# Kernel tuning notes

Measured on AMD Instinct MI355X. Metric: run time of the kernel, lower is better.

The kernel has to match this reference:

```python
import jax, jax.numpy as jnp
import numpy as np

DN = ('NHWC', 'HWIO', 'NHWC')

def conv(x, w, stride=1):
    return jax.lax.conv_general_dilated(x, w, (stride, stride), 'SAME', dimension_numbers=DN)

def up2(x):
    return jnp.repeat(jnp.repeat(x, 2, axis=1), 2, axis=2)

def nms(boxes, scores, max_output=100, iou_thresh=0.5):
    # greedy sequential NMS, fixed trip count, padded outputs
    NEG = jnp.float32(-1e30)
    area = (boxes[:, 2] - boxes[:, 0]) * (boxes[:, 3] - boxes[:, 1])  # [N]
    def step(sw, _):
        idx = jnp.argmax(sw)
        s = sw[idx]
        b = boxes[idx]
        valid = s > NEG * 0.5
        y1 = jnp.maximum(b[0], boxes[:, 0]); x1 = jnp.maximum(b[1], boxes[:, 1])
        y2 = jnp.minimum(b[2], boxes[:, 2]); x2 = jnp.minimum(b[3], boxes[:, 3])
        inter = jnp.maximum(y2 - y1, 0.0) * jnp.maximum(x2 - x1, 0.0)
        barea = (b[2] - b[0]) * (b[3] - b[1])
        iou = inter / (barea + area - inter + 1e-9)
        sw = jnp.where(iou > iou_thresh, NEG, sw)  # suppress (includes self)
        out_b = jnp.where(valid, b, jnp.zeros(4, boxes.dtype))
        out_s = jnp.where(valid, s, jnp.float32(0.0))
        return sw, (out_b, out_s)
    _, (sel_boxes, sel_scores) = jax.lax.scan(step, scores, None, length=max_output)
    return sel_boxes, sel_scores

def setup_inputs() -> dict:
    key = jax.random.key(0)
    ks = jax.random.split(key, 16)
    def w(k, shape):
        fan_in = shape[0] * shape[1] * shape[2]
        return jax.random.normal(k, shape, jnp.float32) * jnp.sqrt(2.0 / fan_in)
    return {
        'inputs': jax.random.normal(ks[0], (1, 512, 512, 3), jnp.float32),
        # backbone (resnet50-style channel widths, strides 2/4/8/16/32)
        'w_stem': w(ks[1], (7, 7, 3, 64)),
        'w_c2': w(ks[2], (3, 3, 64, 256)),
        'w_c3': w(ks[3], (3, 3, 256, 512)),
        'w_c4': w(ks[4], (3, 3, 512, 1024)),
        'w_c5': w(ks[5], (3, 3, 1024, 2048)),
        # FPN laterals + output convs (channels=256)
        'l3': w(ks[6], (1, 1, 512, 256)),
        'l4': w(ks[7], (1, 1, 1024, 256)),
        'l5': w(ks[8], (1, 1, 2048, 256)),
        'o3': w(ks[9], (3, 3, 256, 256)),
        'o4': w(ks[10], (3, 3, 256, 256)),
        'o5': w(ks[11], (3, 3, 256, 256)),
        # RPN: shared 3x3 + obj head (num_anchors=1) + bbox head (4*num_anchors)
        'w_rpn': w(ks[12], (3, 3, 256, 256)),
        'w_obj': w(ks[13], (1, 1, 256, 1)),
        'w_box': w(ks[14], (1, 1, 256, 4)),
    }

def reference(inputs, w_stem, w_c2, w_c3, w_c4, w_c5, l3, l4, l5, o3, o4, o5, w_rpn, w_obj, w_box):
    relu = jax.nn.relu
    # backbone
    s = relu(conv(inputs, w_stem, 2))   # 256x256x64
    c2 = relu(conv(s, w_c2, 2))         # 128x128x256
    c3 = relu(conv(c2, w_c3, 2))        # 64x64x512
    c4 = relu(conv(c3, w_c4, 2))        # 32x32x1024
    c5 = relu(conv(c4, w_c5, 2))        # 16x16x2048
    # FPN
    p5 = conv(c5, l5)
    p4 = conv(c4, l4) + up2(p5)
    p3 = conv(c3, l3) + up2(p4)
    p3, p4, p5 = conv(p3, o3), conv(p4, o4), conv(p5, o5)
    # RPN over all levels (bbox deltas computed per original but unused downstream)
    obj_logits = []
    for p in (p3, p4, p5):
        t = relu(conv(p, w_rpn))
        obj_logits.append(conv(t, w_obj))
        _ = conv(t, w_box)
    obj = obj_logits[0]  # [B, h, w, A]
    B, h, w_, A = obj.shape
    scores = jax.nn.sigmoid(obj).reshape(B, -1)  # [B, h*w*A]
    # anchor grid (fixed 0.1-sized boxes), faithful to TF meshgrid default 'xy' indexing
    yy = jnp.linspace(0.0, 1.0, h)
    xx = jnp.linspace(0.0, 1.0, w_)
    Y, X = jnp.meshgrid(yy, xx)  # shape [w, h]
    boxes = jnp.stack([Y - 0.05, X - 0.05, Y + 0.05, X + 0.05], axis=-1)
    boxes = jnp.clip(boxes, 0.0, 1.0).reshape(-1, 4)  # [w*h, 4]
    sel_boxes, sel_scores = nms(boxes, scores[0], max_output=100, iou_thresh=0.5)
    return sel_boxes, sel_scores
```

## Files before the change

kernel.cpp:

```cpp
#include <hip/hip_runtime.h>
#include <hip/hip_bf16.h>

typedef float f4 __attribute__((ext_vector_type(4)));
typedef short s8v __attribute__((ext_vector_type(8)));
typedef unsigned short us4 __attribute__((ext_vector_type(4)));
typedef unsigned short us8 __attribute__((ext_vector_type(8)));

#define AP 40

__global__ __launch_bounds__(256) void stem_kernel(
    const float* __restrict__ in, const float* __restrict__ w,
    float* __restrict__ out)
{
  __shared__ float in_lds[37 * 37 * 3];
  __shared__ float w_lds[7 * 7 * 3 * 64];
  const int tid = threadIdx.x;
  const int ty0 = (blockIdx.x >> 4) * 16;
  const int tx0 = (blockIdx.x & 15) * 16;

  for (int idx = tid; idx < 9408; idx += 256) w_lds[idx] = w[idx];
  for (int idx = tid; idx < 4107; idx += 256) {
    int ci = idx % 3;
    int rem = idx / 3;
    int ix = rem % 37, iy = rem / 37;
    int gy = ty0 * 2 - 2 + iy, gx = tx0 * 2 - 2 + ix;
    float v = 0.f;
    if ((unsigned)gy < 512u && (unsigned)gx < 512u)
      v = in[(gy * 512 + gx) * 3 + ci];
    in_lds[idx] = v;
  }
  __syncthreads();

  const int co = (tid & 15) * 4;
  const int py = tid >> 4;
  f4 acc[16];
#pragma unroll
  for (int px = 0; px < 16; ++px) acc[px] = (f4)0.f;

  for (int ky = 0; ky < 7; ++ky)
    for (int kx = 0; kx < 7; ++kx)
#pragma unroll
      for (int ci = 0; ci < 3; ++ci) {
        f4 wv = *(const f4*)&w_lds[(((ky * 7 + kx) * 3) + ci) * 64 + co];
        const float* ip = &in_lds[((2 * py + ky) * 37 + kx) * 3 + ci];
#pragma unroll
        for (int px = 0; px < 16; ++px) {
          float iv = ip[px * 6];
          acc[px] += iv * wv;
        }
      }

#pragma unroll
  for (int px = 0; px < 16; ++px) {
    int oy = ty0 + py, ox = tx0 + px;
    f4 o = acc[px];
#pragma unroll
    for (int c = 0; c < 4; ++c) o[c] = fmaxf(o[c], 0.f);
    *(f4*)&out[(oy * 256 + ox) * 64 + co] = o;
  }
}

__global__ __launch_bounds__(256) void wsplit_kernel(
    const float* __restrict__ w, unsigned short* __restrict__ wt,
    int C_in, int C_out, int taps)
{
  __shared__ float t[64][68];
  const int tid = threadIdx.x;
  const int tap = blockIdx.z;
  const int ci0 = blockIdx.x * 64;
  const int co0 = blockIdx.y * 64;
  const size_t lstride = (size_t)taps * C_in * C_out;

#pragma unroll
  for (int q = 0; q < 4; ++q) {
    int f = q * 256 + tid;
    int r = f >> 4, c = f & 15;
    f4 v = *(const f4*)&w[((size_t)(tap * C_in + ci0 + r)) * C_out + co0 + c * 4];
    *(f4*)&t[r][c * 4] = v;
  }
  __syncthreads();

#pragma unroll
  for (int q = 0; q < 4; ++q) {
    int f = q * 256 + tid;
    int r = f >> 4, c = f & 15;
    us4 h, m, l;
#pragma unroll
    for (int u = 0; u < 4; ++u) {
      float s = t[c * 4 + u][r];
      unsigned int ub = __float_as_uint(s);
      unsigned short hh = (unsigned short)(ub >> 16);
      float r1 = s - __uint_as_float((unsigned int)hh << 16);
      unsigned short mm = (unsigned short)(__float_as_uint(r1) >> 16);
      float r2 = r1 - __uint_as_float((unsigned int)mm << 16);
      unsigned short ll = (unsigned short)(__float_as_uint(r2) >> 16);
      h[u] = hh; m[u] = mm; l[u] = ll;
    }
    size_t base = ((size_t)tap * C_out + co0 + r) * C_in + ci0 + c * 4;
    *(us4*)&wt[base] = h;
    *(us4*)&wt[lstride + base] = m;
    *(us4*)&wt[2 * lstride + base] = l;
  }
}

__global__ __launch_bounds__(256, 2) void conv_mfma(
    const float* __restrict__ in, const unsigned short* __restrict__ wt,
    float* __restrict__ pout,
    int H_in, int W_in, int C_in, int wshift, int C_out,
    int stride, int pad, int ci_per_z, int npix, int relu)
{
  __shared__ __align__(16) unsigned short At[3][128][AP];
  __shared__ __align__(16) unsigned short Bt[3][128][AP];
  const int tid = threadIdx.x;

  const int nwg = gridDim.x * gridDim.y * gridDim.z;
  const int hwid = blockIdx.x + gridDim.x * (blockIdx.y + gridDim.y * blockIdx.z);
  const int wid = ((nwg & 7) == 0) ? (hwid & 7) * (nwg >> 3) + (hwid >> 3) : hwid;
  const int bx = wid % gridDim.x;
  const int brem = wid / gridDim.x;
  const int by = brem % gridDim.y;
  const int bz = brem / gridDim.y;

  const int pix_base = bx * 128;
  const int co_base = by * 128;
  const int ci_z0 = bz * ci_per_z;
  const int wmask = (1 << wshift) - 1;
  const size_t lstride = (size_t)9 * C_in * C_out;

  const int lane = tid & 63, wv = tid >> 6;
  const int pixhalf = (wv >> 1) * 64, cohalf = (wv & 1) * 64;
  const int fm = lane & 15, fq = lane >> 4;

  int a_pix[4], a_c4[4], a_ys[4], a_xs[4];
#pragma unroll
  for (int q = 0; q < 4; ++q) {
    int f = q * 256 + tid;
    a_pix[q] = f >> 3; a_c4[q] = f & 7;
    int p = pix_base + a_pix[q];
    a_ys[q] = (p >> wshift) * stride - pad;
    a_xs[q] = (p & wmask) * stride - pad;
  }
  int b_col[2], b_seg[2];
#pragma unroll
  for (int q = 0; q < 2; ++q) {
    int f = q * 256 + tid;
    b_col[q] = f >> 2; b_seg[q] = (f & 3) * 8;
  }

  const int nc = ci_per_z >> 5;
  const int ncsh = nc >> 1;
  const int nchunks = 9 * nc;

  f4 areg[4];
  us8 breg[6];
  auto issue_loads = [&](int c) {
    int tap = c >> ncsh;
    int ci = ci_z0 + (c & (nc - 1)) * 32;
    int ky = tap / 3, kx = tap - ky * 3;
#pragma unroll
    for (int q = 0; q < 4; ++q) {
      int iy = a_ys[q] + ky, ix = a_xs[q] + kx;
      bool v = ((unsigned)iy < (unsigned)H_in) & ((unsigned)ix < (unsigned)W_in);
      const float* p = in + (size_t)(iy * W_in + ix) * C_in + ci + a_c4[q] * 4;
      areg[q] = v ? *(const f4*)p : (f4)0.f;
    }
    const unsigned short* bb =
        wt + (size_t)tap * C_out * C_in + (size_t)co_base * C_in + ci;
#pragma unroll
    for (int L = 0; L < 3; ++L)
#pragma unroll
      for (int q = 0; q < 2; ++q)
        breg[L * 2 + q] = *(const us8*)(bb + (size_t)L * lstride +
                                        (size_t)b_col[q] * C_in + b_seg[q]);
  };

  us4 ah[4], am[4], al[4];
  auto convert = [&]() {
#pragma unroll
    for (int q = 0; q < 4; ++q) {
      f4 s4 = areg[q];
      us4 h, m, l;
#pragma unroll
      for (int u = 0; u < 4; ++u) {
        float s = s4[u];
        unsigned int ub = __float_as_uint(s);
        unsigned short hh = (unsigned short)(ub >> 16);
        float r1 = s - __uint_as_float((unsigned int)hh << 16);
        unsigned short mm = (unsigned short)(__float_as_uint(r1) >> 16);
        float r2 = r1 - __uint_as_float((unsigned int)mm << 16);
        unsigned short ll = (unsigned short)(__float_as_uint(r2) >> 16);
        h[u] = hh; m[u] = mm; l[u] = ll;
      }
      ah[q] = h; am[q] = m; al[q] = l;
    }
  };

  f4 acc[4][4];
#pragma unroll
  for (int i = 0; i < 4; ++i)
#pragma unroll
    for (int j = 0; j < 4; ++j) acc[i][j] = (f4)0.f;

  issue_loads(0);
  convert();

  for (int c = 0; c < nchunks; ++c) {
    __syncthreads();
#pragma unroll
    for (int q = 0; q < 4; ++q) {
      *(us4*)&At[0][a_pix[q]][a_c4[q] * 4] = ah[q];
      *(us4*)&At[1][a_pix[q]][a_c4[q] * 4] = am[q];
      *(us4*)&At[2][a_pix[q]][a_c4[q] * 4] = al[q];
    }
#pragma unroll
    for (int L = 0; L < 3; ++L)
#pragma unroll
      for (int q = 0; q < 2; ++q)
        *(us8*)&Bt[L][b_col[q]][b_seg[q]] = breg[L * 2 + q];
    __syncthreads();

    const bool more = (c + 1 < nchunks);
    if (more) issue_loads(c + 1);

    s8v Bh[4], Bm[4], Bl[4];
#pragma unroll
    for (int j = 0; j < 4; ++j) {
      Bh[j] = *(const s8v*)&Bt[0][cohalf + j * 16 + fm][fq * 8];
      Bm[j] = *(const s8v*)&Bt[1][cohalf + j * 16 + fm][fq * 8];
      Bl[j] = *(const s8v*)&Bt[2][cohalf + j * 16 + fm][fq * 8];
    }
    {
      s8v Ah[4];
#pragma unroll
      for (int i = 0; i < 4; ++i)
        Ah[i] = *(const s8v*)&At[0][pixhalf + i * 16 + fm][fq * 8];
#pragma unroll
      for (int i = 0; i < 4; ++i)
#pragma unroll
        for (int j = 0; j < 4; ++j) {
          acc[i][j] = __builtin_amdgcn_mfma_f32_16x16x32_bf16(Ah[i], Bh[j], acc[i][j], 0, 0, 0);
          acc[i][j] = __builtin_amdgcn_mfma_f32_16x16x32_bf16(Ah[i], Bm[j], acc[i][j], 0, 0, 0);
          acc[i][j] = __builtin_amdgcn_mfma_f32_16x16x32_bf16(Ah[i], Bl[j], acc[i][j], 0, 0, 0);
        }
    }
    {
      s8v Am[4];
#pragma unroll
      for (int i = 0; i < 4; ++i)
        Am[i] = *(const s8v*)&At[1][pixhalf + i * 16 + fm][fq * 8];
#pragma unroll
      for (int i = 0; i < 4; ++i)
#pragma unroll
        for (int j = 0; j < 4; ++j) {
          acc[i][j] = __builtin_amdgcn_mfma_f32_16x16x32_bf16(Am[i], Bh[j], acc[i][j], 0, 0, 0);
          acc[i][j] = __builtin_amdgcn_mfma_f32_16x16x32_bf16(Am[i], Bm[j], acc[i][j], 0, 0, 0);
        }
    }
    {
      s8v Al[4];
#pragma unroll
      for (int i = 0; i < 4; ++i)
        Al[i] = *(const s8v*)&At[2][pixhalf + i * 16 + fm][fq * 8];
#pragma unroll
      for (int i = 0; i < 4; ++i)
#pragma unroll
        for (int j = 0; j < 4; ++j)
          acc[i][j] = __builtin_amdgcn_mfma_f32_16x16x32_bf16(Al[i], Bh[j], acc[i][j], 0, 0, 0);
    }

    if (more) convert();
  }

  float* dst = pout + (size_t)bz * npix * C_out;
#pragma unroll
  for (int i = 0; i < 4; ++i) {
#pragma unroll
    for (int j = 0; j < 4; ++j) {
#pragma unroll
      for (int r = 0; r < 4; ++r) {
        int p = pix_base + pixhalf + i * 16 + fq * 4 + r;
        int co = co_base + cohalf + j * 16 + fm;
        float v = acc[i][j][r];
        if (relu) v = fmaxf(v, 0.f);
        dst[(size_t)p * C_out + co] = v;
      }
    }
  }
}

__global__ __launch_bounds__(256) void reduce_relu_kernel(
    const float* __restrict__ p, float* __restrict__ out, int n4, int Z, int relu)
{
  int idx = blockIdx.x * 256 + threadIdx.x;
  if (idx >= n4) return;
  const f4* pv = (const f4*)p;
  f4 s = pv[idx];
  for (int z = 1; z < Z; ++z) s += pv[(size_t)z * n4 + idx];
  if (relu) {
#pragma unroll
    for (int c = 0; c < 4; ++c) s[c] = fmaxf(s[c], 0.f);
  }
  ((f4*)out)[idx] = s;
}

__global__ __launch_bounds__(256) void gemm64(
    const float* __restrict__ in, const float* __restrict__ w,
    float* __restrict__ pout, int C_in, int C_out, int ci_per_z, int npix)
{
  __shared__ __align__(16) float As2[32][68];
  __shared__ __align__(16) float Bs[32][64];
  const int tid = threadIdx.x;
  const int pix_base = blockIdx.x * 64;
  const int co_base = blockIdx.y * 64;
  const int ci_z0 = blockIdx.z * ci_per_z;
  const int tx = tid & 15, ty = tid >> 4;

  int ga_pix[2], ga_c4[2];
#pragma unroll
  for (int q = 0; q < 2; ++q) {
    int f = q * 256 + tid;
    ga_pix[q] = f >> 3; ga_c4[q] = f & 7;
  }
  int gb_row[2], gb_c4[2];
#pragma unroll
  for (int q = 0; q < 2; ++q) {
    int f = q * 256 + tid;
    gb_row[q] = f >> 4; gb_c4[q] = f & 15;
  }

  f4 acc[4];
#pragma unroll
  for (int i = 0; i < 4; ++i) acc[i] = (f4)0.f;

  for (int ci = ci_z0; ci < ci_z0 + ci_per_z; ci += 32) {
    __syncthreads();
#pragma unroll
    for (int q = 0; q < 2; ++q) {
      f4 av = *(const f4*)&in[(size_t)(pix_base + ga_pix[q]) * C_in + ci + ga_c4[q] * 4];
#pragma unroll
      for (int u = 0; u < 4; ++u) As2[ga_c4[q] * 4 + u][ga_pix[q]] = av[u];
    }
#pragma unroll
    for (int q = 0; q < 2; ++q) {
      *(f4*)&Bs[gb_row[q]][gb_c4[q] * 4] =
          *(const f4*)&w[(size_t)(ci + gb_row[q]) * C_out + co_base + gb_c4[q] * 4];
    }
    __syncthreads();
#pragma unroll
    for (int kk = 0; kk < 32; ++kk) {
      f4 a = *(const f4*)&As2[kk][ty * 4];
      f4 b = *(const f4*)&Bs[kk][tx * 4];
#pragma unroll
      for (int i = 0; i < 4; ++i) acc[i] += a[i] * b;
    }
  }

  float* dst = pout + (size_t)blockIdx.z * npix * C_out;
#pragma unroll
  for (int i = 0; i < 4; ++i)
    *(f4*)&dst[(size_t)(pix_base + ty * 4 + i) * C_out + co_base + tx * 4] = acc[i];
}

__global__ __launch_bounds__(256) void reduce_up2_kernel(
    const float* __restrict__ p, const float* __restrict__ res,
    float* __restrict__ out, int n4, int Z, int wshift)
{
  int idx = blockIdx.x * 256 + threadIdx.x;
  if (idx >= n4) return;
  const f4* pv = (const f4*)p;
  f4 s = pv[idx];
  for (int z = 1; z < Z; ++z) s += pv[(size_t)z * n4 + idx];
  if (res) {
    int pix = idx >> 6, c4 = idx & 63;
    int oy = pix >> wshift, ox = pix & ((1 << wshift) - 1);
    int rp = ((oy >> 1) << (wshift - 1)) + (ox >> 1);
    s += ((const f4*)res)[rp * 64 + c4];
  }
  ((f4*)out)[idx] = s;
}

__global__ __launch_bounds__(256) void obj_sigmoid_kernel(
    const float* __restrict__ t, const float* __restrict__ wobj,
    float* __restrict__ scores)
{
  __shared__ float wl[256];
  const int tid = threadIdx.x;
  wl[tid] = wobj[tid];
  __syncthreads();
  const int pix = blockIdx.x * 64 + (tid >> 2);
  const int c0 = (tid & 3) * 64;
  float acc = 0.f;
#pragma unroll
  for (int k = 0; k < 16; ++k) {
    f4 tv = *(const f4*)&t[(size_t)pix * 256 + c0 + k * 4];
    const float* wp = &wl[c0 + k * 4];
    acc += tv[0] * wp[0] + tv[1] * wp[1] + tv[2] * wp[2] + tv[3] * wp[3];
  }
  acc += __shfl_xor(acc, 1);
  acc += __shfl_xor(acc, 2);
  if ((tid & 3) == 0) scores[pix] = 1.f / (1.f + expf(-acc));
}

__global__ __launch_bounds__(1024) void nms_kernel(
    const float* __restrict__ scores, float* __restrict__ out)
{
  __shared__ unsigned long long keys[4096];
  __shared__ float acc_lds[100 * 8];
  const int tid = threadIdx.x;
  const float inv63 = 1.0f / 63.0f;

  if (tid < 125) ((f4*)out)[tid] = (f4)0.f;

#pragma unroll
  for (int r = 0; r < 4; ++r) {
    int idx = r * 1024 + tid;
    unsigned int bits = __float_as_uint(scores[idx]);
    keys[idx] = ((unsigned long long)(0x40000000u - bits) << 16) |
                (unsigned long long)idx;
  }

  int prev_cross = 1;
  for (int k = 2; k <= 4096; k <<= 1) {
    for (int j = k >> 1; j > 0; j >>= 1) {
      const int cross = (j > 32);
      if (cross | prev_cross) {
        __syncthreads();
      } else {
        asm volatile("s_waitcnt lgkmcnt(0)" ::: "memory");
      }
#pragma unroll
      for (int q = 0; q < 2; ++q) {
        int p = q * 1024 + tid;
        int i = ((p & ~(j - 1)) << 1) | (p & (j - 1));
        int partner = i | j;
        bool up = ((i & k) == 0);
        unsigned long long a = keys[i], b = keys[partner];
        if ((a > b) == up) { keys[i] = b; keys[partner] = a; }
      }
      prev_cross = cross;
    }
  }
  __syncthreads();

  if (tid >= 64) return;
  const int lane = tid;

  int n = 0;
  for (int b = 0; b < 64 && n < 100; ++b) {
    unsigned long long kk = keys[b * 64 + lane];
    int idx = (int)(kk & 0xFFFF);
    float sc = __uint_as_float(0x40000000u - (unsigned int)(kk >> 16));
    int si = idx >> 6, sj = idx & 63;
    float y = sj * inv63, x = si * inv63;
    float c0 = fmaxf(y - 0.05f, 0.f), c1 = fmaxf(x - 0.05f, 0.f);
    float c2 = fminf(y + 0.05f, 1.f), c3 = fminf(x + 0.05f, 1.f);
    float carea = (c2 - c0) * (c3 - c1);

    bool sup = false;
    for (int a = 0; a < n; ++a) {
      f4 ab = *(const f4*)&acc_lds[a * 8];
      float aarea = acc_lds[a * 8 + 4];
      float yy1 = fmaxf(ab[0], c0), xx1 = fmaxf(ab[1], c1);
      float yy2 = fminf(ab[2], c2), xx2 = fminf(ab[3], c3);
      float inter = fmaxf(yy2 - yy1, 0.f) * fmaxf(xx2 - xx1, 0.f);
      float iou = inter / (aarea + carea - inter + 1e-9f);
      sup = sup || (iou > 0.5f);
    }

    unsigned long long m = __ballot(!sup);
    while (m != 0 && n < 100) {
      int u = __builtin_ctzll(m);
      float b0 = __shfl(c0, u), b1 = __shfl(c1, u);
      float b2 = __shfl(c2, u), b3 = __shfl(c3, u);
      float ba = __shfl(carea, u);
      if (lane == u) {
        acc_lds[n * 8 + 0] = c0; acc_lds[n * 8 + 1] = c1;
        acc_lds[n * 8 + 2] = c2; acc_lds[n * 8 + 3] = c3;
        acc_lds[n * 8 + 4] = carea;
        out[n * 4 + 0] = c0; out[n * 4 + 1] = c1;
        out[n * 4 + 2] = c2; out[n * 4 + 3] = c3;
        out[400 + n] = sc;
        sup = true;
      }
      n++;
      if (lane > u && !sup) {
        float yy1 = fmaxf(b0, c0), xx1 = fmaxf(b1, c1);
        float yy2 = fminf(b2, c2), xx2 = fminf(b3, c3);
        float inter = fmaxf(yy2 - yy1, 0.f) * fmaxf(xx2 - xx1, 0.f);
        float iou = inter / (ba + carea - inter + 1e-9f);
        if (iou > 0.5f) sup = true;
      }
      m = __ballot(!sup);
    }
    __threadfence_block();
  }
}

extern "C" void kernel_launch(void* const* d_in, const int* in_sizes, int n_in,
                              void* d_out, int out_size, void* d_ws, size_t ws_size,
                              hipStream_t stream) {
  const float* x      = (const float*)d_in[0];
  const float* w_stem = (const float*)d_in[1];
  const float* w_c2   = (const float*)d_in[2];
  const float* w_c3   = (const float*)d_in[3];
  const float* w_c4   = (const float*)d_in[4];
  const float* w_c5   = (const float*)d_in[5];
  const float* l3     = (const float*)d_in[6];
  const float* l4     = (const float*)d_in[7];
  const float* l5     = (const float*)d_in[8];
  const float* o3w    = (const float*)d_in[9];
  const float* w_rpn  = (const float*)d_in[12];
  const float* w_obj  = (const float*)d_in[13];
  float* out = (float*)d_out;
  float* ws = (float*)d_ws;

  float* S   = ws;
  float* C2  = S   + 4194304;
  float* C3  = C2  + 4194304;
  float* C4  = C3  + 2097152;
  float* C5  = C4  + 1048576;
  float* P5  = C5  + 524288;
  float* P4  = P5  + 65536;
  float* P3P = P4  + 262144;
  float* P3  = P3P + 1048576;
  float* T   = P3  + 1048576;
  float* SC  = T   + 1048576;
  unsigned short* WT = (unsigned short*)(SC + 4096);
  float* PZ = (float*)(WT + 31457280);

  stem_kernel<<<256, 256, 0, stream>>>(x, w_stem, S);

  wsplit_kernel<<<dim3(1, 4, 9), 256, 0, stream>>>(w_c2, WT, 64, 256, 9);
  conv_mfma<<<dim3(128, 2, 2), 256, 0, stream>>>(
      S, WT, PZ, 256, 256, 64, 7, 256, 2, 0, 32, 16384, 0);
  reduce_relu_kernel<<<4096, 256, 0, stream>>>(PZ, C2, 1048576, 2, 1);

  wsplit_kernel<<<dim3(4, 8, 9), 256, 0, stream>>>(w_c3, WT, 256, 512, 9);
  conv_mfma<<<dim3(32, 4, 4), 256, 0, stream>>>(
      C2, WT, PZ, 128, 128, 256, 6, 512, 2, 0, 64, 4096, 0);
  reduce_relu_kernel<<<2048, 256, 0, stream>>>(PZ, C3, 524288, 4, 1);

  wsplit_kernel<<<dim3(8, 16, 9), 256, 0, stream>>>(w_c4, WT, 512, 1024, 9);
  conv_mfma<<<dim3(8, 8, 8), 256, 0, stream>>>(
      C3, WT, S, 64, 64, 512, 5, 1024, 2, 0, 64, 1024, 0);
  reduce_relu_kernel<<<1024, 256, 0, stream>>>(S, C4, 262144, 8, 1);

  wsplit_kernel<<<dim3(16, 32, 9), 256, 0, stream>>>(w_c5, WT, 1024, 2048, 9);
  conv_mfma<<<dim3(2, 16, 16), 256, 0, stream>>>(
      C4, WT, S, 32, 32, 1024, 4, 2048, 2, 0, 64, 256, 0);
  reduce_relu_kernel<<<512, 256, 0, stream>>>(S, C5, 131072, 16, 1);

  gemm64<<<dim3(4, 4, 8), 256, 0, stream>>>(C5, l5, S, 2048, 256, 256, 256);
  reduce_up2_kernel<<<64, 256, 0, stream>>>(S, nullptr, P5, 16384, 8, 4);
  gemm64<<<dim3(16, 4, 4), 256, 0, stream>>>(C4, l4, S, 1024, 256, 256, 1024);
  reduce_up2_kernel<<<256, 256, 0, stream>>>(S, P5, P4, 65536, 4, 5);
  gemm64<<<dim3(64, 4, 2), 256, 0, stream>>>(C3, l3, S, 512, 256, 256, 4096);
  reduce_up2_kernel<<<1024, 256, 0, stream>>>(S, P4, P3P, 262144, 2, 6);

  wsplit_kernel<<<dim3(4, 4, 9), 256, 0, stream>>>(o3w, WT, 256, 256, 9);
  conv_mfma<<<dim3(32, 2, 8), 256, 0, stream>>>(
      P3P, WT, S, 64, 64, 256, 6, 256, 1, 1, 32, 4096, 0);
  reduce_relu_kernel<<<1024, 256, 0, stream>>>(S, P3, 262144, 8, 0);

  wsplit_kernel<<<dim3(4, 4, 9), 256, 0, stream>>>(w_rpn, WT, 256, 256, 9);
  conv_mfma<<<dim3(32, 2, 8), 256, 0, stream>>>(
      P3, WT, S, 64, 64, 256, 6, 256, 1, 1, 32, 4096, 0);
  reduce_relu_kernel<<<1024, 256, 0, stream>>>(S, T, 262144, 8, 1);

  obj_sigmoid_kernel<<<64, 256, 0, stream>>>(T, w_obj, SC);
  nms_kernel<<<1, 1024, 0, stream>>>(SC, out);
}
```

Before: 640.6 us.

## Register-resident bitonic sort in NMS using shuffles for small strides

Rewrites the bitonic sort in the NMS kernel so each thread holds four keys in registers. Stages with stride 4 to 128 use cross-lane shuffles, strides 1 and 2 are compared inside the thread, and only strides of 256 or more go through LDS with barriers. This is meant to cut the many LDS round-trips and block-wide syncs of the old shared-memory sort. The tradeoff is that 64-bit shuffles take two instructions each and register use goes up.

```diff
diff --git a/kernel.cpp b/kernel.cpp
--- a/kernel.cpp
+++ b/kernel.cpp
@@ -411,35 +411,75 @@
 
   if (tid < 125) ((f4*)out)[tid] = (f4)0.f;
 
-#pragma unroll
-  for (int r = 0; r < 4; ++r) {
-    int idx = r * 1024 + tid;
-    unsigned int bits = __float_as_uint(scores[idx]);
-    keys[idx] = ((unsigned long long)(0x40000000u - bits) << 16) |
-                (unsigned long long)idx;
-  }
-
-  int prev_cross = 1;
+  unsigned long long kr[4];
+  {
+    f4 sv = ((const f4*)scores)[tid];
+#pragma unroll
+    for (int v = 0; v < 4; ++v) {
+      unsigned int bits = __float_as_uint(sv[v]);
+      kr[v] = ((unsigned long long)(0x40000000u - bits) << 16) |
+              (unsigned long long)(tid * 4 + v);
+    }
+  }
+
   for (int k = 2; k <= 4096; k <<= 1) {
-    for (int j = k >> 1; j > 0; j >>= 1) {
-      const int cross = (j > 32);
-      if (cross | prev_cross) {
-        __syncthreads();
-      } else {
-        asm volatile("s_waitcnt lgkmcnt(0)" ::: "memory");
-      }
-#pragma unroll
-      for (int q = 0; q < 2; ++q) {
-        int p = q * 1024 + tid;
-        int i = ((p & ~(j - 1)) << 1) | (p & (j - 1));
-        int partner = i | j;
-        bool up = ((i & k) == 0);
-        unsigned long long a = keys[i], b = keys[partner];
-        if ((a > b) == up) { keys[i] = b; keys[partner] = a; }
-      }
-      prev_cross = cross;
-    }
-  }
+    for (int j = k >> 1; j >= 256; j >>= 1) {
+      *(ulonglong2*)&keys[tid * 4] = ulonglong2{kr[0], kr[1]};
+      *(ulonglong2*)&keys[tid * 4 + 2] = ulonglong2{kr[2], kr[3]};
+      __syncthreads();
+      ulonglong2 p0 = *(const ulonglong2*)&keys[(tid * 4) ^ j];
+      ulonglong2 p1 = *(const ulonglong2*)&keys[((tid * 4) ^ j) + 2];
+      unsigned long long pb[4] = {p0.x, p0.y, p1.x, p1.y};
+#pragma unroll
+      for (int v = 0; v < 4; ++v) {
+        int e = tid * 4 + v;
+        bool up = ((e & k) == 0);
+        bool lower = ((e & j) == 0);
+        bool keep_min = (lower == up);
+        unsigned long long a = kr[v], b = pb[v];
+        unsigned long long mn = a < b ? a : b;
+        unsigned long long mx = a < b ? b : a;
+        kr[v] = keep_min ? mn : mx;
+      }
+      __syncthreads();
+    }
+    {
+      int js = (k >> 1) < 128 ? (k >> 1) : 128;
+      for (int j = js; j >= 4; j >>= 1) {
+        int lm = j >> 2;
+        bool lower = ((tid & lm) == 0);
+        bool up = ((tid & (k >> 2)) == 0);
+        bool keep_min = (lower == up);
+#pragma unroll
+        for (int v = 0; v < 4; ++v) {
+          unsigned long long b = __shfl_xor(kr[v], lm);
+          unsigned long long a = kr[v];
+          unsigned long long mn = a < b ? a : b;
+          unsigned long long mx = a < b ? b : a;
+          kr[v] = keep_min ? mn : mx;
+        }
+      }
+    }
+    if (k >= 4) {
+#pragma unroll
+      for (int v = 0; v < 2; ++v) {
+        bool up = (((tid * 4 + v) & k) == 0);
+        unsigned long long a = kr[v], b = kr[v + 2];
+        if ((a > b) == up) { kr[v] = b; kr[v + 2] = a; }
+      }
+    }
+    {
+#pragma unroll
+      for (int v = 0; v < 4; v += 2) {
+        bool up = (((tid * 4 + v) & k) == 0);
+        unsigned long long a = kr[v], b = kr[v + 1];
+        if ((a > b) == up) { kr[v] = b; kr[v + 1] = a; }
+      }
+    }
+  }
+
+  *(ulonglong2*)&keys[tid * 4] = ulonglong2{kr[0], kr[1]};
+  *(ulonglong2*)&keys[tid * 4 + 2] = ulonglong2{kr[2], kr[3]};
   __syncthreads();
 
   if (tid >= 64) return;
```

New measurement: 664.3 us. 1.04x slower.
